# Optimization experiments

Measured on AMD Instinct MI355X. Metric: run time of the kernel, lower is better.

## Reference

```python
import jax, jax.numpy as jnp
import numpy as np
import math

B, LL, LP, H, C, S, T = 16, 512, 2048, 1024, 8192, 10, 4
PAD_TOKEN_ID = 2000
VAR_TOKEN_BASE = 2001


def _attend(q, k, v):
    # q: [b,q,h], k/v: [b,k,h]
    scores = jnp.einsum('bqh,bkh->bqk', q, k) / math.sqrt(float(q.shape[-1]))
    w = jax.nn.softmax(scores, axis=-1)
    return jnp.einsum('bqk,bkh->bqh', w, v)


def _gru_cell(x, h, Wih, Whh, bih, bhh):
    gi = x @ Wih + bih   # [B,3H], gate order r,z,n (torch GRUCell)
    gh = h @ Whh + bhh
    i_r, i_z, i_n = jnp.split(gi, 3, axis=-1)
    h_r, h_z, h_n = jnp.split(gh, 3, axis=-1)
    r = jax.nn.sigmoid(i_r + h_r)
    z = jax.nn.sigmoid(i_z + h_z)
    n = jnp.tanh(i_n + r * h_n)
    return (1.0 - z) * n + z * h


def setup_inputs() -> dict:
    key = jax.random.key(0)
    ks = jax.random.split(key, 18)
    def lin(k, i, o):
        return jax.random.normal(k, (i, o), jnp.float32) * 0.02
    return {
        'logic_hidden': jax.random.normal(ks[0], (B, LL, H), jnp.float32),
        'prompt_hidden': jax.random.normal(ks[1], (B, LP, H), jnp.float32),
        'codebook_emb': jax.random.normal(ks[2], (C, H), jnp.float32) * 0.02,
        'W_init': lin(ks[3], 2 * H, H),
        'W_pq': lin(ks[4], H, H),
        'W_pk': lin(ks[5], H, H),
        'W_pv': lin(ks[6], H, H),
        'slot_queries': jax.random.normal(ks[7], (S - 1, H), jnp.float32) * 0.02,
        'W_sq': lin(ks[8], H, H),
        'W_op': lin(ks[9], H, H),
        'W_gate': lin(ks[10], H, 1),
        'b_gate': jnp.zeros((1,), jnp.float32),
        'W_stop': lin(ks[11], 2 * H, 1),
        'b_stop': jnp.zeros((1,), jnp.float32),
        'gru_Wih': lin(ks[12], H, 3 * H),
        'gru_Whh': lin(ks[13], H, 3 * H),
        'gru_bih': jnp.zeros((3 * H,), jnp.float32),
        'gru_bhh': jnp.zeros((3 * H,), jnp.float32),
    }


def reference(logic_hidden, prompt_hidden, codebook_emb, W_init, W_pq, W_pk, W_pv,
              slot_queries, W_sq, W_op, W_gate, b_gate, W_stop, b_stop,
              gru_Wih, gru_Whh, gru_bih, gru_bhh):
    batch = logic_hidden.shape[0]
    prompt_summary = prompt_hidden.mean(axis=1)
    logic_summary = logic_hidden.mean(axis=1)
    state = jnp.tanh(jnp.concatenate([prompt_summary, logic_summary], axis=-1) @ W_init)
    pk = prompt_hidden @ W_pk   # [B,LP,H]
    pv = prompt_hidden @ W_pv
    cb_sq = jnp.sum(codebook_emb * codebook_emb, axis=-1)   # [C]
    slot_idx = jnp.arange(S - 1, dtype=jnp.int64)[None, :].repeat(batch, axis=0)

    summaries, stop_logits, stop_probs = [], [], []
    for _ in range(T):
        state_q = (state @ W_pq)[:, None, :]
        state_ctx = _attend(state_q, pk, pv)[:, 0, :]         # [B,H]
        op_pre = state_ctx @ W_op
        # squared euclidean distance to codebook without [B,C,H] diff tensor
        dist = (jnp.sum(op_pre * op_pre, axis=-1, keepdims=True)
                - 2.0 * (op_pre @ codebook_emb.T) + cb_sq[None, :])  # [B,C]
        op_logits = -dist
        op_idx = jnp.argmax(op_logits, axis=-1)               # [B]
        op_embedding = codebook_emb[op_idx]                   # [B,H]
        slot_seed = state_ctx[:, None, :] + slot_queries[None, :, :]   # [B,S-1,H]
        slot_q = slot_seed @ W_sq
        slot_tensors = _attend(slot_q, pk, pv)                # [B,S-1,H]
        slot_use_probs = jax.nn.sigmoid((slot_seed @ W_gate)[..., 0] + b_gate[0])  # [B,S-1]
        slot_mask = slot_use_probs >= 0.5
        # fallback if no slot selected anywhere in the batch (global check, as in torch)
        fb_mask = jax.nn.one_hot(jnp.argmax(slot_use_probs, axis=-1), S - 1, dtype=jnp.bool_)
        slot_mask = jnp.where(jnp.any(slot_mask), slot_mask, fb_mask)
        mf = slot_mask.astype(slot_tensors.dtype)
        slot_summary = jnp.sum(slot_tensors * mf[..., None], axis=1) / \
            jnp.clip(jnp.sum(mf, axis=-1, keepdims=True), 1.0)
        matrix_summary = jnp.tanh(op_embedding + slot_summary)
        stop_logit = (jnp.concatenate([state_ctx, matrix_summary], axis=-1) @ W_stop)[:, 0] + b_stop[0]
        summaries.append(matrix_summary)
        stop_logits.append(stop_logit)
        stop_probs.append(jax.nn.sigmoid(stop_logit))
        state = _gru_cell(matrix_summary, state, gru_Wih, gru_Whh, gru_bih, gru_bhh)

    stop_logits_t = jnp.stack(stop_logits, axis=1)   # [B,T]
    stop_probs_t = jnp.stack(stop_probs, axis=1)
    summary_stack = jnp.stack(summaries, axis=1)     # [B,T,H]
    stop_hits = stop_probs_t >= 0.5
    chain_lengths = jnp.argmax(stop_hits.astype(jnp.int64), axis=1) + 1
    chain_lengths = jnp.where(jnp.sum(stop_hits, axis=1) == 0,
                              jnp.full_like(chain_lengths, T), chain_lengths)
    return summary_stack, stop_logits_t, stop_probs_t, chain_lengths
```

## Files before the change

kernel.cpp:

```cpp
#include <hip/hip_runtime.h>


#define DINL __device__ __forceinline__

DINL float dot4(float4 a, float4 b) {
  return fmaf(a.x, b.x, fmaf(a.y, b.y, fmaf(a.z, b.z, a.w * b.w)));
}
DINL unsigned sortable(float f) {
  unsigned u = __float_as_uint(f);
  return (u & 0x80000000u) ? ~u : (u | 0x80000000u);
}
#define AXPY4(A, W, P) \
  { A.x = fmaf(W, P.x, A.x); A.y = fmaf(W, P.y, A.y); A.z = fmaf(W, P.z, A.z); A.w = fmaf(W, P.w, A.w); }
#define ADD4(A, V) { A.x += V.x; A.y += V.y; A.z += V.z; A.w += V.w; }

static constexpr int F_CBSQ  = 0;
static constexpr int F_STATE = 8192;
static constexpr int F_WQK   = 24576;
static constexpr int F_T1    = F_WQK + 1048576;
static constexpr int F_WFUSE = F_T1 + 1048576;
static constexpr int F_SQKCP = F_WFUSE + 2105344;
static constexpr int F_E     = F_SQKCP + 36928;
static constexpr int F_UN    = F_E + 294912;
static constexpr int F_PMP   = F_UN;
static constexpr int F_LMP   = F_PMP + 1048576;
static constexpr int F_MEAN  = F_LMP + 262144;
static constexpr int F_S2P   = F_MEAN + 32768;
static constexpr int F_WQKP  = F_UN;
static constexpr int F_T1P   = F_UN + 4194304;
static constexpr int F_WFP   = F_UN;
static constexpr int F_QS1   = F_UN;
static constexpr int F_LST   = F_QS1 + 131072;
static constexpr int F_CTX   = F_LST + 4096;
static constexpr int F_FWP   = F_CTX + 16384;
static constexpr int F_OPV   = F_FWP + 1052672;
static constexpr int F_OPMAX = F_OPV + 16384;
static constexpr int F_OPIDX = F_OPMAX + 16384;
static constexpr int F_GPRE  = F_OPIDX + 64;
static constexpr int F_GC    = F_GPRE + 64;
static constexpr int F_STOPA = F_GC + 64;
static constexpr int F_QSLB  = F_STOPA + 64;
static constexpr int F_LPS   = F_QSLB + 16384;
static constexpr int F_SSUM  = F_LPS + 4672;
static constexpr int F_MS    = F_SSUM + 16384;
static constexpr int F_GP    = F_MS + 16384;
static constexpr int F_K8P   = F_GP + 786432;
static constexpr int F_BIG   = F_K8P + 262144;

struct SG {
  const float* Bm;
  const float* Bg;
  const float* a0;
  float* out;
  int M, N, Ncore, NB, kslice, ksh, lda, ldb, ldo, mr;
  float scale;
};

template <int MR>
DINL void sgemm_body(const SG p, int bx, float* As) {
  const int t = threadIdx.x;
  const int ks = bx / p.NB, nb = bx % p.NB;
  const int kslice = p.kslice;
  const int kb = ks * kslice;
  const int tot = p.M * kslice;
  for (int idx = t; idx < tot; idx += 256) {
    const int m = idx >> p.ksh;
    const int kl = idx & (kslice - 1);
    As[(m << p.ksh) + kl] = p.a0[m * p.lda + kb + kl];
  }
  __syncthreads();
  const int nl = t & 63, mg = t >> 6;
  const int n = nb * 64 + nl;
  const bool nok = (n < p.N);
  float acc[MR];
#pragma unroll
  for (int i = 0; i < MR; i++) acc[i] = 0.f;
  const bool useg = nok && (n >= p.Ncore);
  const float* Bc = p.Bm + n;
  for (int k4 = 0; k4 < kslice; k4 += 4) {
    float bv[4];
#pragma unroll
    for (int u = 0; u < 4; u++) {
      bv[u] = 0.f;
      if (nok) bv[u] = useg ? p.Bg[kb + k4 + u] : Bc[(kb + k4 + u) * p.ldb];
    }
#pragma unroll
    for (int i = 0; i < MR; i++) {
      const int m = mg + 4 * i;
      if (MR == 4 || m < p.M) {
        const float4 av = *(const float4*)&As[(m << p.ksh) + k4];
        acc[i] = fmaf(av.x, bv[0], acc[i]);
        acc[i] = fmaf(av.y, bv[1], acc[i]);
        acc[i] = fmaf(av.z, bv[2], acc[i]);
        acc[i] = fmaf(av.w, bv[3], acc[i]);
      }
    }
  }
  if (nok) {
#pragma unroll
    for (int i = 0; i < MR; i++) {
      const int m = mg + 4 * i;
      if (MR == 4 || m < p.M) p.out[(ks * p.M + m) * p.ldo + n] = acc[i] * p.scale;
    }
  }
}

__global__ __launch_bounds__(256) void k_sgemm(SG p) {
  __shared__ __align__(16) float As[4352];
  if (p.mr == 4) sgemm_body<4>(p, blockIdx.x, As);
  else sgemm_body<7>(p, blockIdx.x, As);
}

DINL int sw4(int c) { return c ^ (((c >> 5) & 3) << 2); }

__global__ __launch_bounds__(256) void k_wgT(const float* __restrict__ A1,
                                             const float* __restrict__ B,
                                             float* __restrict__ C1P,
                                             const float* __restrict__ A2,
                                             float* __restrict__ C2P) {
  __shared__ __align__(16) float As[16 * 132], Bs[16 * 132];
  const int bx = blockIdx.x;
  const int which = bx >> 8;
  const int rem = bx & 255;
  const int ks = rem >> 6;
  const int tile = rem & 63;
  const int bi = tile >> 3, bj = tile & 7;
  const float* A = which ? A2 : A1;
  float* CP = (which ? C2P : C1P) + ks * 1048576;
  const int t = threadIdx.x;
  const int sr = t >> 2, q4 = t & 3;
  const int tr = (t >> 4) << 3, tc = (t & 15) << 3;
  const int stc0 = sw4(tc), stc1 = sw4(tc + 4);
  float acc[8][8];
#pragma unroll
  for (int i = 0; i < 8; i++)
#pragma unroll
    for (int j = 0; j < 8; j++) acc[i][j] = 0.f;

  const int k00 = ks * 256;
  for (int k0 = k00; k0 < k00 + 256; k0 += 16) {
    __syncthreads();
#pragma unroll
    for (int h = 0; h < 2; h++) {
      const int r = sr + h * 64;
      const float4 av = *(const float4*)&A[(bi * 128 + r) * 1024 + k0 + q4 * 4];
      const float4 bv = *(const float4*)&B[(bj * 128 + r) * 1024 + k0 + q4 * 4];
      As[(q4 * 4 + 0) * 132 + r] = av.x; As[(q4 * 4 + 1) * 132 + r] = av.y;
      As[(q4 * 4 + 2) * 132 + r] = av.z; As[(q4 * 4 + 3) * 132 + r] = av.w;
      const int swr = sw4(r);
      Bs[(q4 * 4 + 0) * 132 + swr] = bv.x; Bs[(q4 * 4 + 1) * 132 + swr] = bv.y;
      Bs[(q4 * 4 + 2) * 132 + swr] = bv.z; Bs[(q4 * 4 + 3) * 132 + swr] = bv.w;
    }
    __syncthreads();
#pragma unroll
    for (int kk = 0; kk < 16; kk++) {
      const float* ar = &As[kk * 132];
      const float* br = &Bs[kk * 132];
      const float4 a0 = *(const float4*)&ar[tr];
      const float4 a1 = *(const float4*)&ar[tr + 4];
      const float4 b0 = *(const float4*)&br[stc0];
      const float4 b1 = *(const float4*)&br[stc1];
      const float a[8] = {a0.x, a0.y, a0.z, a0.w, a1.x, a1.y, a1.z, a1.w};
      const float b[8] = {b0.x, b0.y, b0.z, b0.w, b1.x, b1.y, b1.z, b1.w};
#pragma unroll
      for (int i = 0; i < 8; i++)
#pragma unroll
        for (int j = 0; j < 8; j++) acc[i][j] = fmaf(a[i], b[j], acc[i][j]);
    }
  }
#pragma unroll
  for (int i = 0; i < 8; i++) {
    const int row = bi * 128 + tr + i;
    *(float4*)&CP[row * 1024 + bj * 128 + tc] =
        make_float4(acc[i][0], acc[i][1], acc[i][2], acc[i][3]);
    *(float4*)&CP[row * 1024 + bj * 128 + tc + 4] =
        make_float4(acc[i][4], acc[i][5], acc[i][6], acc[i][7]);
  }
}

__global__ __launch_bounds__(256) void k_combT(const float* __restrict__ C1P,
                                               const float* __restrict__ C2P,
                                               float* __restrict__ C1,
                                               float* __restrict__ C2, float scale) {
  const int bx = blockIdx.x;
  const int half = bx >> 12;
  const int i = ((bx & 4095) << 8) + threadIdx.x;
  const float* src = half ? C2P : C1P;
  float s = 0.f;
#pragma unroll
  for (int ks = 0; ks < 4; ks++) s += src[ks * 1048576 + i];
  (half ? C2 : C1)[i] = s * scale;
}

__global__ __launch_bounds__(256) void k_wgF(const float* __restrict__ Wpv,
                                             const float* __restrict__ Wop,
                                             const float* __restrict__ T1,
                                             float* __restrict__ CfP) {
  __shared__ __align__(16) float As[16 * 132], Bs[16 * 132];
  const int bx = blockIdx.x;
  const int ks = bx >> 7;
  const int rem = bx & 127;
  const int bi = rem >> 4, bj = rem & 15;
  const float* Bsrc = (bj < 8) ? (Wop + bj * 128) : (T1 + (bj - 8) * 128);
  float* CP = CfP + ks * 2105344;
  const int t = threadIdx.x;
  const int sr = t >> 2, q4 = t & 3;
  const int kkq = t >> 4, c8 = (t & 15) << 3;
  const int tr = (t >> 4) << 3, tc = (t & 15) << 3;
  const int stc0 = sw4(tc), stc1 = sw4(tc + 4);
  float acc[8][8];
#pragma unroll
  for (int i = 0; i < 8; i++)
#pragma unroll
    for (int j = 0; j < 8; j++) acc[i][j] = 0.f;

  const int k00 = ks * 256;
  for (int k0 = k00; k0 < k00 + 256; k0 += 16) {
    __syncthreads();
#pragma unroll
    for (int h = 0; h < 2; h++) {
      const int r = sr + h * 64;
      const float4 av = *(const float4*)&Wpv[(bi * 128 + r) * 1024 + k0 + q4 * 4];
      As[(q4 * 4 + 0) * 132 + r] = av.x; As[(q4 * 4 + 1) * 132 + r] = av.y;
      As[(q4 * 4 + 2) * 132 + r] = av.z; As[(q4 * 4 + 3) * 132 + r] = av.w;
    }
    {
      const float4 v0 = *(const float4*)&Bsrc[(k0 + kkq) * 1024 + c8];
      const float4 v1 = *(const float4*)&Bsrc[(k0 + kkq) * 1024 + c8 + 4];
      *(float4*)&Bs[kkq * 132 + sw4(c8)] = v0;
      *(float4*)&Bs[kkq * 132 + sw4(c8 + 4)] = v1;
    }
    __syncthreads();
#pragma unroll
    for (int kk = 0; kk < 16; kk++) {
      const float* ar = &As[kk * 132];
      const float* br = &Bs[kk * 132];
      const float4 a0 = *(const float4*)&ar[tr];
      const float4 a1 = *(const float4*)&ar[tr + 4];
      const float4 b0 = *(const float4*)&br[stc0];
      const float4 b1 = *(const float4*)&br[stc1];
      const float a[8] = {a0.x, a0.y, a0.z, a0.w, a1.x, a1.y, a1.z, a1.w};
      const float b[8] = {b0.x, b0.y, b0.z, b0.w, b1.x, b1.y, b1.z, b1.w};
#pragma unroll
      for (int i = 0; i < 8; i++)
#pragma unroll
        for (int j = 0; j < 8; j++) acc[i][j] = fmaf(a[i], b[j], acc[i][j]);
    }
  }
#pragma unroll
  for (int i = 0; i < 8; i++) {
    const int row = bi * 128 + tr + i;
    *(float4*)&CP[row * 2056 + bj * 128 + tc] =
        make_float4(acc[i][0], acc[i][1], acc[i][2], acc[i][3]);
    *(float4*)&CP[row * 2056 + bj * 128 + tc + 4] =
        make_float4(acc[i][4], acc[i][5], acc[i][6], acc[i][7]);
  }
}

__global__ __launch_bounds__(256) void k_combF(const float* __restrict__ CfP,
                                               float* __restrict__ Cf) {
  const int i2 = blockIdx.x * 256 + threadIdx.x;
  const int r = i2 >> 11, c = i2 & 2047;
  float s = 0.f;
#pragma unroll
  for (int ks = 0; ks < 4; ks++) s += CfP[ks * 2105344 + r * 2056 + c];
  Cf[r * 2056 + c] = s;
}

__global__ __launch_bounds__(256) void k_gs(const float* __restrict__ Wpv,
                                            const float* __restrict__ Wgate,
                                            const float* __restrict__ Wstop,
                                            float* __restrict__ Cf) {
  const int t = threadIdx.x;
  const int row = blockIdx.x * 16 + (t >> 4);
  const int lane = t & 15;
  const float* base = Wpv + row * 1024 + lane * 64;
  const float* gb = Wgate + lane * 64;
  const float* sb = Wstop + lane * 64;
  float g = 0.f, s = 0.f;
#pragma unroll 4
  for (int k = 0; k < 64; k += 4) {
    const float4 av = *(const float4*)&base[k];
    const float4 gv = *(const float4*)&gb[k];
    const float4 sv = *(const float4*)&sb[k];
    g += dot4(av, gv);
    s += dot4(av, sv);
  }
#pragma unroll
  for (int off = 8; off > 0; off >>= 1) {
    g += __shfl_xor(g, off);
    s += __shfl_xor(s, off);
  }
  if (lane == 0) {
    Cf[row * 2056 + 2048] = g;
    Cf[row * 2056 + 2049] = s;
  }
}

__global__ __launch_bounds__(512) void k_E(const float* __restrict__ prompt,
                                           const float* __restrict__ sqkcP,
                                           float* __restrict__ E) {
  __shared__ __align__(16) char qsm[36864];
  const int b = blockIdx.y, kc = blockIdx.x;
  const int t = threadIdx.x;
  for (int idx = t; idx < 9216; idx += 512) {
    const int j = idx >> 10, h = idx & 1023;
    float s = 0.f;
    for (int sp = 0; sp < 4; sp++) s += sqkcP[(sp * 9 + j) * 1025 + h];
    const int x = idx << 2;
    *(float*)(qsm + (x ^ (((x >> 7) & 7) << 4))) = s;
  }
  __syncthreads();
  const int w = t >> 6, l = t & 63;
  const int bxl = 64 * l;
  const int key = ((bxl >> 7) & 7) << 4;
  const int o0 = bxl ^ key, o1 = (bxl + 16) ^ key, o2 = (bxl + 32) ^ key, o3 = (bxl + 48) ^ key;
  const int k0 = kc * 64 + w * 8;
  const float* pbase = prompt + ((b * 2048 + k0) << 10) + 16 * l;
  for (int ki = 0; ki < 8; ki++) {
    const float4* pr = (const float4*)(pbase + (ki << 10));
    const float4 p0 = pr[0], p1 = pr[1], p2 = pr[2], p3 = pr[3];
    float sj[9];
#pragma unroll
    for (int j = 0; j < 9; j++) {
      const char* qp = qsm + (j << 12);
      sj[j] = dot4(*(const float4*)(qp + o0), p0) + dot4(*(const float4*)(qp + o1), p1) +
              dot4(*(const float4*)(qp + o2), p2) + dot4(*(const float4*)(qp + o3), p3);
    }
#pragma unroll
    for (int off = 32; off > 0; off >>= 1) {
#pragma unroll
      for (int j = 0; j < 9; j++) sj[j] += __shfl_xor(sj[j], off);
    }
    float wv = sj[0];
#pragma unroll
    for (int j = 1; j < 9; j++)
      if (l == j) wv = sj[j];
    if (l < 9) E[(b * 2048 + k0 + ki) * 9 + l] = __expf(wv);
  }
}

__global__ __launch_bounds__(256) void k_meanpsum(const float* __restrict__ src,
                                                  float* __restrict__ out, int rpc) {
  const int s = blockIdx.x, b = blockIdx.y, t = threadIdx.x;
  const int R = gridDim.x * rpc;
  const float4* base = (const float4*)src + (size_t)(b * R + s * rpc) * 256 + t;
  float4 acc = make_float4(0.f, 0.f, 0.f, 0.f);
#pragma unroll 4
  for (int r = 0; r < rpc; r++) {
    const float4 v = base[r * 256];
    ADD4(acc, v);
  }
  ((float4*)out)[((s * 16 + b) << 8) + t] = acc;
}

__global__ __launch_bounds__(256) void k_cbsq(const float* __restrict__ cbv,
                                              float* __restrict__ out) {
  const int c = blockIdx.x * 4 + (threadIdx.x >> 6);
  const int l = threadIdx.x & 63;
  const float4* cr = (const float4*)(cbv + (c << 10));
  float s = 0.f;
#pragma unroll
  for (int r = 0; r < 4; r++) {
    const float4 v = cr[4 * l + r];
    s += dot4(v, v);
  }
#pragma unroll
  for (int off = 32; off > 0; off >>= 1) s += __shfl_xor(s, off);
  if (l == 0) out[c] = s;
}

__global__ __launch_bounds__(256) void k_meancat(const float* __restrict__ pmp,
                                                 const float* __restrict__ lmp,
                                                 float* __restrict__ mean) {
  const int gi = blockIdx.x * 256 + threadIdx.x;
  const int b = gi >> 11, k = gi & 2047;
  float v = 0.f;
  if (k < 1024) {
    for (int s = 0; s < 64; s++) v += pmp[((s * 16 + b) << 10) + k];
    v *= (1.f / 2048.f);
  } else {
    const int kk = k - 1024;
    for (int s = 0; s < 16; s++) v += lmp[((s * 16 + b) << 10) + kk];
    v *= (1.f / 512.f);
  }
  mean[b * 2048 + k] = v;
}

__global__ __launch_bounds__(256) void k_s2b(const float* __restrict__ s2p,
                                             float* __restrict__ state) {
  const int gi = blockIdx.x * 256 + threadIdx.x;
  const int b = gi >> 10, h = gi & 1023;
  float s = 0.f;
  for (int si = 0; si < 8; si++) s += s2p[((si * 16 + b) << 10) + h];
  state[gi] = tanhf(s);
}


DINL void ph_qs1(int bx, char* smemc, const float* state, const float* Wqk,
                 float* outP) {
  float* As = (float*)smemc;
  const int t = threadIdx.x;
  const int ks = bx >> 4, nb = bx & 15;
  const int kb = ks * 128;
  for (int idx = t; idx < 2048; idx += 256)
    As[idx] = state[((idx >> 7) << 10) + kb + (idx & 127)];
  __syncthreads();
  const int nl = t & 63, mg = t >> 6;
  const int n = nb * 64 + nl;
  const float* Bc = Wqk + n;
  float acc[4] = {0.f, 0.f, 0.f, 0.f};
  for (int k4 = 0; k4 < 128; k4 += 4) {
    float bv[4];
#pragma unroll
    for (int u = 0; u < 4; u++) bv[u] = Bc[(kb + k4 + u) << 10];
#pragma unroll
    for (int i = 0; i < 4; i++) {
      const float4 av = *(const float4*)&As[((mg + 4 * i) << 7) + k4];
      acc[i] = fmaf(av.x, bv[0], acc[i]);
      acc[i] = fmaf(av.y, bv[1], acc[i]);
      acc[i] = fmaf(av.z, bv[2], acc[i]);
      acc[i] = fmaf(av.w, bv[3], acc[i]);
    }
  }
#pragma unroll
  for (int i = 0; i < 4; i++)
    outP[((ks * 16 + mg + 4 * i) << 10) + n] = acc[i];
}

DINL void ph_flash(int vb, const float* prompt, const float* qs1P,
                   float* accst, float* lst) {
  const int b = vb >> 6;
  const int w = threadIdx.x >> 6, l = threadIdx.x & 63;
  const int chunk = (vb & 63) * 4 + w;
  float4 q0 = make_float4(0.f, 0.f, 0.f, 0.f), q1 = q0, q2 = q0, q3 = q0;
#pragma unroll
  for (int s = 0; s < 8; s++) {
    const float4* qp = (const float4*)(qs1P + ((s * 16 + b) << 10) + 16 * l);
    ADD4(q0, qp[0]); ADD4(q1, qp[1]); ADD4(q2, qp[2]); ADD4(q3, qp[3]);
  }
  float4 acc[4];
#pragma unroll
  for (int r = 0; r < 4; r++) acc[r] = make_float4(0.f, 0.f, 0.f, 0.f);
  float lsum = 0.f;
  const float* pbase = prompt + ((b * 2048 + chunk * 8) << 10) + 16 * l;
#pragma unroll 2
  for (int k = 0; k < 8; k++) {
    const float4* pr = (const float4*)(pbase + (k << 10));
    const float4 p0 = pr[0], p1 = pr[1], p2 = pr[2], p3 = pr[3];
    float s = dot4(q0, p0) + dot4(q1, p1) + dot4(q2, p2) + dot4(q3, p3);
#pragma unroll
    for (int off = 32; off > 0; off >>= 1) s += __shfl_xor(s, off);
    const float wgt = __expf(s);
    lsum += wgt;
    AXPY4(acc[0], wgt, p0); AXPY4(acc[1], wgt, p1);
    AXPY4(acc[2], wgt, p2); AXPY4(acc[3], wgt, p3);
  }
  float* ob = accst + ((chunk * 16 + b) << 10) + 16 * l;
#pragma unroll
  for (int r = 0; r < 4; r++) ((float4*)ob)[r] = acc[r];
  if (l == 0) lst[chunk * 16 + b] = lsum;
}

DINL void ph_cst(int bx, char* smemc, const float* accst, const float* lst,
                 float* ctx) {
  float4* sred = (float4*)smemc;
  float* rinvp = (float*)(smemc + 4096);
  const int b = bx >> 4, hq = bx & 15;
  const int t = threadIdx.x;
  if (t < 64) {
    float s = 0.f;
    for (int c = t; c < 256; c += 64) s += lst[c * 16 + b];
#pragma unroll
    for (int off = 32; off > 0; off >>= 1) s += __shfl_xor(s, off);
    if (t == 0) rinvp[0] = 1.f / s;
  }
  const int h4 = hq * 16 + (t & 15);
  const int cp = t >> 4;
  float4 a = make_float4(0.f, 0.f, 0.f, 0.f);
#pragma unroll
  for (int ci = 0; ci < 16; ci++) {
    const int c = cp * 16 + ci;
    const float4 v = ((const float4*)accst)[((c * 16 + b) << 8) + h4];
    ADD4(a, v);
  }
  sred[t] = a;
  __syncthreads();
  if (t < 16) {
    float4 s = sred[t];
    for (int p2 = 1; p2 < 16; p2++) {
      const float4 v = sred[p2 * 16 + t];
      ADD4(s, v);
    }
    const float rinv = rinvp[0];
    s.x *= rinv; s.y *= rinv; s.z *= rinv; s.w *= rinv;
    ((float4*)ctx)[(b << 8) + hq * 16 + t] = s;
  }
}

DINL void ph_fw(int bx, char* smemc, const float* ctx, const float* wfuse,
                float* outp) {
  float* As = (float*)smemc;
  const int t = threadIdx.x;
  const int ks = bx / 33, nb = bx % 33;
  const int kb = ks * 64;
  for (int idx = t; idx < 1024; idx += 256)
    As[idx] = ctx[((idx >> 6) << 10) + kb + (idx & 63)];
  __syncthreads();
  const int nl = t & 63, mg = t >> 6;
  const int n = nb * 64 + nl;
  const bool nok = (n < 2050);
  const float* Bc = wfuse + n;
  float acc[4] = {0.f, 0.f, 0.f, 0.f};
  for (int k4 = 0; k4 < 64; k4 += 4) {
    float bv[4];
#pragma unroll
    for (int u = 0; u < 4; u++) bv[u] = nok ? Bc[(kb + k4 + u) * 2056] : 0.f;
#pragma unroll
    for (int i = 0; i < 4; i++) {
      const float4 av = *(const float4*)&As[((mg + 4 * i) << 6) + k4];
      acc[i] = fmaf(av.x, bv[0], acc[i]);
      acc[i] = fmaf(av.y, bv[1], acc[i]);
      acc[i] = fmaf(av.z, bv[2], acc[i]);
      acc[i] = fmaf(av.w, bv[3], acc[i]);
    }
  }
  if (nok) {
#pragma unroll
    for (int i = 0; i < 4; i++) outp[(ks * 16 + mg + 4 * i) * 2056 + n] = acc[i];
  }
}

DINL void ph_combw(int bx, const float* fwP, const float* sqkcP, float* opv,
                   float* qslb, float* gpre, float* gc, float* stopA) {
  const int t = threadIdx.x;
  if (bx < 64) {
    const int i = bx * 256 + t;
    const int b = i >> 10, h = i & 1023;
    float s = 0.f;
    for (int p = 0; p < 16; p++) s += fwP[(p * 16 + b) * 2056 + h];
    opv[i] = s;
  } else if (bx < 128) {
    const int i = (bx - 64) * 256 + t;
    const int b = i >> 10, h = i & 1023;
    float s = 0.f;
    for (int p = 0; p < 16; p++) s += fwP[(p * 16 + b) * 2056 + 1024 + h];
    qslb[i] = s;
  } else {
    if (t < 16) {
      float g = 0.f, sa = 0.f;
      for (int p = 0; p < 16; p++) {
        g += fwP[(p * 16 + t) * 2056 + 2048];
        sa += fwP[(p * 16 + t) * 2056 + 2049];
      }
      gpre[t] = g;
      stopA[t] = sa;
    } else if (t < 25) {
      const int j = t - 16;
      float g = 0.f;
      for (int sp = 0; sp < 4; sp++) g += sqkcP[(sp * 9 + j) * 1025 + 1024];
      gc[j] = g;
    }
  }
}

DINL void ph_slot(int vb, char* smemc, const float* prompt, const float* qslb,
// ... 224 lines not shown
  const int kb = ks * 128;
  for (int idx = t; idx < 2048; idx += 256) {
    const int m = idx >> 7, kl = idx & 127;
    float v;
    if (!half) {
      float s = 0.f;
      for (int p = 0; p < 16; p++) s += k8p[((p * 16 + m) << 10) + kb + kl];
      v = tanhf(s + cbv[(opidx[m] << 10) + kb + kl]);
      if (nb == 0) {
        ms[(m << 10) + kb + kl] = v;
        dout[(m << 12) + (it << 10) + kb + kl] = v;
      }
    } else {
      v = state[(m << 10) + kb + kl];
    }
    As[idx] = v;
  }
  __syncthreads();
  const int nl = t & 63, mg = t >> 6;
  const int n = nb * 64 + nl;
  const float* Bc = (half ? Whh : Wih) + n;
  float acc[4] = {0.f, 0.f, 0.f, 0.f};
  for (int k4 = 0; k4 < 128; k4 += 4) {
    float bv[4];
#pragma unroll
    for (int u = 0; u < 4; u++) bv[u] = Bc[(kb + k4 + u) * 3072];
#pragma unroll
    for (int i = 0; i < 4; i++) {
      const float4 av = *(const float4*)&As[((mg + 4 * i) << 7) + k4];
      acc[i] = fmaf(av.x, bv[0], acc[i]);
      acc[i] = fmaf(av.y, bv[1], acc[i]);
      acc[i] = fmaf(av.z, bv[2], acc[i]);
      acc[i] = fmaf(av.w, bv[3], acc[i]);
    }
  }
  float* outp = gpP + half * 3072;
#pragma unroll
  for (int i = 0; i < 4; i++) outp[(ks * 16 + mg + 4 * i) * 6144 + n] = acc[i];
}

DINL void ph_k9b(int bx, const float* gp, const float* bih, const float* bhh,
                 float* state, const float* stopA, const float* ms,
                 const float* Wstop, const float* bstop, float* dout, int it) {
  const int t = threadIdx.x;
  if (bx < 64) {
    const int gi = bx * 256 + t;
    const int b = gi >> 10, h = gi & 1023;
    float ir = 0.f, iz = 0.f, inn = 0.f, hr = 0.f, hz = 0.f, hn = 0.f;
    for (int s = 0; s < 8; s++) {
      const float* g = gp + (s * 16 + b) * 6144;
      ir += g[h]; iz += g[1024 + h]; inn += g[2048 + h];
      hr += g[3072 + h]; hz += g[4096 + h]; hn += g[5120 + h];
    }
    ir += bih[h]; iz += bih[1024 + h]; inn += bih[2048 + h];
    hr += bhh[h]; hz += bhh[1024 + h]; hn += bhh[2048 + h];
    const float r = 1.f / (1.f + __expf(-(ir + hr)));
    const float z = 1.f / (1.f + __expf(-(iz + hz)));
    const float n = tanhf(fmaf(r, hn, inn));
    const float hold = state[gi];
    state[gi] = (1.f - z) * n + z * hold;
  } else {
    const int wid = (bx - 64) * 4 + (t >> 6);
    const int l = t & 63;
    float p = 0.f;
    for (int i = 0; i < 16; i++) {
      const int h = l + (i << 6);
      p = fmaf(ms[(wid << 10) + h], Wstop[1024 + h], p);
    }
#pragma unroll
    for (int off = 32; off > 0; off >>= 1) p += __shfl_xor(p, off);
    if (l == 0) {
      const float lg = p + stopA[wid] + bstop[0];
      dout[65536 + wid * 4 + it] = lg;
      dout[65600 + wid * 4 + it] = 1.f / (1.f + __expf(-lg));
    }
  }
}

__global__ __launch_bounds__(256) void kf_qs1(const float* state, const float* Wqk, float* outP) {
  __shared__ __align__(16) char smem[8192];
  ph_qs1(blockIdx.x, smem, state, Wqk, outP);
}
__global__ __launch_bounds__(256) void kf_flash(const float* prompt, const float* qs1P,
                                                float* accst, float* lst) {
  ph_flash(blockIdx.x, prompt, qs1P, accst, lst);
}
__global__ __launch_bounds__(256) void kf_cst(const float* accst, const float* lst, float* ctx) {
  __shared__ __align__(16) char smem[4112];
  ph_cst(blockIdx.x, smem, accst, lst, ctx);
}
__global__ __launch_bounds__(256) void kf_fw(const float* ctx, const float* wfuse, float* outp) {
  __shared__ __align__(16) char smem[4096];
  ph_fw(blockIdx.x, smem, ctx, wfuse, outp);
}
__global__ __launch_bounds__(256) void kf_combw(const float* fwP, const float* sqkcP,
                                                float* opv, float* qslb, float* gpre,
                                                float* gc, float* stopA) {
  ph_combw(blockIdx.x, fwP, sqkcP, opv, qslb, gpre, gc, stopA);
}
__global__ __launch_bounds__(256) void k_slotcb(const float* prompt, const float* qslb,
                                                const float* E, float* accp, float* lpsum,
                                                const float* opv, const float* cbv,
                                                const float* cbsqv,
                                                unsigned long long* opmaxp) {
  __shared__ __align__(16) char smem[33024];
  const int bx = blockIdx.x;
  if (bx < 512) ph_slot(bx, smem, prompt, qslb, E, accp, lpsum);
  else ph_cb(bx - 512, smem, opv, cbv, cbsqv, opmaxp);
}
__global__ __launch_bounds__(256) void kf_k7(const float* accp, const float* lpsum,
                                             const float* gpre_g, const float* gc_g,
                                             const float* bgate,
                                             const unsigned long long* opmax,
                                             int* opidx, float* ssum) {
  __shared__ __align__(16) char smem[2304];
  ph_k7(blockIdx.x, smem, accp, lpsum, gpre_g, gc_g, bgate, opmax, opidx, ssum);
}
__global__ __launch_bounds__(256) void kf_k8p(const float* ssum, const float* Wpv, float* outP) {
  __shared__ __align__(16) char smem[4096];
  ph_k8p(blockIdx.x, smem, ssum, Wpv, outP);
}
__global__ __launch_bounds__(256) void kf_gru(const float* k8p, const int* opidx,
                                              const float* cbv, const float* state,
                                              const float* Wih, const float* Whh,
                                              float* gpP, float* ms, float* dout, int it) {
  __shared__ __align__(16) char smem[8192];
  ph_gru(blockIdx.x, smem, k8p, opidx, cbv, state, Wih, Whh, gpP, ms, dout, it);
}
__global__ __launch_bounds__(256) void kf_k9b(const float* gp, const float* bih,
                                              const float* bhh, float* state,
                                              const float* stopA, const float* ms,
                                              const float* Wstop, const float* bstop,
                                              float* dout, int it) {
  ph_k9b(blockIdx.x, gp, bih, bhh, state, stopA, ms, Wstop, bstop, dout, it);
}
__global__ void kf_k10(float* __restrict__ dout) {
  const int t = threadIdx.x;
  if (t < 16) {
    int cl = 4;
    for (int it = 0; it < 4; it++) {
      if (dout[65536 + t * 4 + it] >= 0.f) { cl = it + 1; break; }
    }
    dout[65664 + t] = (float)cl;
  }
}

static SG baseSG() {
  SG p;
  p.Bm = nullptr; p.Bg = nullptr; p.a0 = nullptr; p.out = nullptr;
  p.M = 16; p.N = 1024; p.Ncore = 1024;
  p.NB = 16; p.kslice = 64; p.ksh = 6;
  p.lda = 1024; p.ldb = 1024; p.ldo = 1024;
  p.mr = 4; p.scale = 1.f;
  return p;
}

extern "C" void kernel_launch(void* const* d_in, const int* in_sizes, int n_in,
                              void* d_out, int out_size, void* d_ws, size_t ws_size,
                              hipStream_t stream) {
  (void)in_sizes; (void)n_in; (void)out_size; (void)ws_size;
  const float* logic  = (const float*)d_in[0];
  const float* prompt = (const float*)d_in[1];
  const float* cbv    = (const float*)d_in[2];
  const float* W_init = (const float*)d_in[3];
  const float* W_pq   = (const float*)d_in[4];
  const float* W_pk   = (const float*)d_in[5];
  const float* W_pv   = (const float*)d_in[6];
  const float* slotq  = (const float*)d_in[7];
  const float* W_sq   = (const float*)d_in[8];
  const float* W_op   = (const float*)d_in[9];
  const float* W_gate = (const float*)d_in[10];
  const float* b_gate = (const float*)d_in[11];
  const float* W_stop = (const float*)d_in[12];
  const float* b_stop = (const float*)d_in[13];
  const float* Wih    = (const float*)d_in[14];
  const float* Whh    = (const float*)d_in[15];
  const float* bih    = (const float*)d_in[16];
  const float* bhh    = (const float*)d_in[17];
  float* out = (float*)d_out;
  float* w = (float*)d_ws;

  const float inv32 = 1.0f / 32.0f;

  k_meanpsum<<<dim3(64, 16), 256, 0, stream>>>(prompt, w + F_PMP, 32);
  k_meanpsum<<<dim3(16, 16), 256, 0, stream>>>(logic, w + F_LMP, 32);
  k_cbsq<<<2048, 256, 0, stream>>>(cbv, w + F_CBSQ);
  k_gs<<<64, 256, 0, stream>>>(W_pv, W_gate, W_stop, w + F_WFUSE);
  k_meancat<<<128, 256, 0, stream>>>(w + F_PMP, w + F_LMP, w + F_MEAN);
  {
    SG p = baseSG();
    p.a0 = w + F_MEAN; p.Bm = W_init; p.out = w + F_S2P;
    p.kslice = 256; p.ksh = 8; p.lda = 2048; p.NB = 16;
    k_sgemm<<<128, 256, 0, stream>>>(p);
  }
  k_s2b<<<64, 256, 0, stream>>>(w + F_S2P, w + F_STATE);
  k_wgT<<<512, 256, 0, stream>>>(W_pq, W_pk, w + F_WQKP, W_sq, w + F_T1P);
  k_combT<<<8192, 256, 0, stream>>>(w + F_WQKP, w + F_T1P, w + F_WQK, w + F_T1, inv32);
  {
    SG p = baseSG();
    p.a0 = slotq; p.Bm = w + F_T1; p.Bg = W_gate;
    p.M = 9; p.N = 1025; p.Ncore = 1024; p.NB = 17;
    p.kslice = 256; p.ksh = 8; p.out = w + F_SQKCP; p.ldo = 1025; p.mr = 7;
    k_sgemm<<<68, 256, 0, stream>>>(p);
  }
  k_E<<<dim3(32, 16), 512, 0, stream>>>(prompt, w + F_SQKCP, w + F_E);
  k_wgF<<<512, 256, 0, stream>>>(W_pv, W_op, w + F_T1, w + F_WFP);
  k_combF<<<8192, 256, 0, stream>>>(w + F_WFP, w + F_WFUSE);

  for (int it = 0; it < 4; ++it) {
    kf_qs1<<<128, 256, 0, stream>>>(w + F_STATE, w + F_WQK, w + F_QS1);
    kf_flash<<<1024, 256, 0, stream>>>(prompt, w + F_QS1, w + F_BIG, w + F_LST);
    kf_cst<<<256, 256, 0, stream>>>(w + F_BIG, w + F_LST, w + F_CTX);
    kf_fw<<<528, 256, 0, stream>>>(w + F_CTX, w + F_WFUSE, w + F_FWP);
    kf_combw<<<129, 256, 0, stream>>>(w + F_FWP, w + F_SQKCP, w + F_OPV,
                                      w + F_QSLB, w + F_GPRE, w + F_GC, w + F_STOPA);
    k_slotcb<<<1024, 256, 0, stream>>>(prompt, w + F_QSLB, w + F_E,
                                       w + F_BIG, w + F_LPS, w + F_OPV, cbv,
                                       w + F_CBSQ,
                                       (unsigned long long*)(w + F_OPMAX));
    kf_k7<<<65, 256, 0, stream>>>(w + F_BIG, w + F_LPS, w + F_GPRE, w + F_GC,
                                  b_gate, (const unsigned long long*)(w + F_OPMAX),
                                  (int*)(w + F_OPIDX), w + F_SSUM);
    kf_k8p<<<256, 256, 0, stream>>>(w + F_SSUM, W_pv, w + F_K8P);
    kf_gru<<<768, 256, 0, stream>>>(w + F_K8P, (const int*)(w + F_OPIDX), cbv,
                                    w + F_STATE, Wih, Whh, w + F_GP, w + F_MS,
                                    out, it);
    kf_k9b<<<68, 256, 0, stream>>>(w + F_GP, bih, bhh, w + F_STATE, w + F_STOPA,
                                   w + F_MS, W_stop, b_stop, out, it);
  }
  kf_k10<<<1, 64, 0, stream>>>(out);
}
```

Measured before the change: 900.9 us.

## Merge setup kernels into four multi-phase launches and reduce flash partials in-block

The setup kernels that can run together (weight GEMM partials, means, codebook norms, gate sums, combines, E) are merged into four launches that dispatch on block index ranges. The workspace gets non-aliased regions so the merged phases cannot overwrite each other's buffers. The flash kernel now sums its four waves' partial accumulators in shared memory before writing, which shrinks the partial buffer and the reduction work in kf_cst. This removes launch gaps and per-iteration global traffic, at the cost of mixed register and LDS usage per merged kernel and a larger workspace.

```diff
diff --git a/kernel.cpp b/kernel.cpp
--- a/kernel.cpp
+++ b/kernel.cpp
@@ -15,25 +15,25 @@
 #define ADD4(A, V) { A.x += V.x; A.y += V.y; A.z += V.z; A.w += V.w; }
 
 static constexpr int F_CBSQ  = 0;
-static constexpr int F_STATE = 8192;
-static constexpr int F_WQK   = 24576;
+static constexpr int F_STATE = F_CBSQ + 8192;
+static constexpr int F_WQK   = F_STATE + 16384;
 static constexpr int F_T1    = F_WQK + 1048576;
 static constexpr int F_WFUSE = F_T1 + 1048576;
 static constexpr int F_SQKCP = F_WFUSE + 2105344;
 static constexpr int F_E     = F_SQKCP + 36928;
-static constexpr int F_UN    = F_E + 294912;
-static constexpr int F_PMP   = F_UN;
+static constexpr int F_PMP   = F_E + 294912;
 static constexpr int F_LMP   = F_PMP + 1048576;
 static constexpr int F_MEAN  = F_LMP + 262144;
 static constexpr int F_S2P   = F_MEAN + 32768;
-static constexpr int F_WQKP  = F_UN;
-static constexpr int F_T1P   = F_UN + 4194304;
-static constexpr int F_WFP   = F_UN;
-static constexpr int F_QS1   = F_UN;
-static constexpr int F_LST   = F_QS1 + 131072;
-static constexpr int F_CTX   = F_LST + 4096;
+static constexpr int F_WQKP  = F_S2P + 131072;
+static constexpr int F_T1P   = F_WQKP + 4194304;
+static constexpr int F_WFP   = F_T1P + 4194304;
+static constexpr int F_QS1   = F_WFP + 8421376;
+static constexpr int F_ACCSM = F_QS1 + 131072;
+static constexpr int F_LSM   = F_ACCSM + 1048576;
+static constexpr int F_CTX   = F_LSM + 1024;
 static constexpr int F_FWP   = F_CTX + 16384;
-static constexpr int F_OPV   = F_FWP + 1052672;
+static constexpr int F_OPV   = F_FWP + 526336;
 static constexpr int F_OPMAX = F_OPV + 16384;
 static constexpr int F_OPIDX = F_OPMAX + 16384;
 static constexpr int F_GPRE  = F_OPIDX + 64;
@@ -45,7 +45,7 @@
 static constexpr int F_MS    = F_SSUM + 16384;
 static constexpr int F_GP    = F_MS + 16384;
 static constexpr int F_K8P   = F_GP + 786432;
-static constexpr int F_BIG   = F_K8P + 262144;
+static constexpr int F_ACCP  = F_K8P + 262144;
 
 struct SG {
   const float* Bm;
@@ -105,21 +105,13 @@
   }
 }
 
-__global__ __launch_bounds__(256) void k_sgemm(SG p) {
-  __shared__ __align__(16) float As[4352];
-  if (p.mr == 4) sgemm_body<4>(p, blockIdx.x, As);
-  else sgemm_body<7>(p, blockIdx.x, As);
-}
-
 DINL int sw4(int c) { return c ^ (((c >> 5) & 3) << 2); }
 
-__global__ __launch_bounds__(256) void k_wgT(const float* __restrict__ A1,
-                                             const float* __restrict__ B,
-                                             float* __restrict__ C1P,
-                                             const float* __restrict__ A2,
-                                             float* __restrict__ C2P) {
-  __shared__ __align__(16) float As[16 * 132], Bs[16 * 132];
-  const int bx = blockIdx.x;
+DINL void ph_wgT(int bx, float* sm, const float* __restrict__ A1,
+                 const float* __restrict__ B, float* __restrict__ C1P,
+                 const float* __restrict__ A2, float* __restrict__ C2P) {
+  float* As = sm;
+  float* Bs = sm + 2112;
   const int which = bx >> 8;
   const int rem = bx & 255;
   const int ks = rem >> 6;
@@ -178,26 +170,11 @@
   }
 }
 
-__global__ __launch_bounds__(256) void k_combT(const float* __restrict__ C1P,
-                                               const float* __restrict__ C2P,
-                                               float* __restrict__ C1,
-                                               float* __restrict__ C2, float scale) {
-  const int bx = blockIdx.x;
-  const int half = bx >> 12;
-  const int i = ((bx & 4095) << 8) + threadIdx.x;
-  const float* src = half ? C2P : C1P;
-  float s = 0.f;
-#pragma unroll
-  for (int ks = 0; ks < 4; ks++) s += src[ks * 1048576 + i];
-  (half ? C2 : C1)[i] = s * scale;
-}
-
-__global__ __launch_bounds__(256) void k_wgF(const float* __restrict__ Wpv,
-                                             const float* __restrict__ Wop,
-                                             const float* __restrict__ T1,
-                                             float* __restrict__ CfP) {
-  __shared__ __align__(16) float As[16 * 132], Bs[16 * 132];
-  const int bx = blockIdx.x;
+DINL void ph_wgF(int bx, float* sm, const float* __restrict__ Wpv,
+                 const float* __restrict__ Wop, const float* __restrict__ T1,
+                 float* __restrict__ CfP) {
+  float* As = sm;
+  float* Bs = sm + 2112;
   const int ks = bx >> 7;
   const int rem = bx & 127;
   const int bi = rem >> 4, bj = rem & 15;
@@ -257,22 +234,38 @@
   }
 }
 
-__global__ __launch_bounds__(256) void k_combF(const float* __restrict__ CfP,
-                                               float* __restrict__ Cf) {
-  const int i2 = blockIdx.x * 256 + threadIdx.x;
-  const int r = i2 >> 11, c = i2 & 2047;
+DINL void ph_meanpsum(int vb, const float* __restrict__ src,
+                      float* __restrict__ out, int R) {
+  const int s = vb >> 4, b = vb & 15, t = threadIdx.x;
+  const float4* base = (const float4*)src + (size_t)(b * R + s * 32) * 256 + t;
+  float4 acc = make_float4(0.f, 0.f, 0.f, 0.f);
+#pragma unroll 4
+  for (int r = 0; r < 32; r++) {
+    const float4 v = base[r * 256];
+    ADD4(acc, v);
+  }
+  ((float4*)out)[((s * 16 + b) << 8) + t] = acc;
+}
+
+DINL void ph_cbsq(int vb, const float* __restrict__ cbv, float* __restrict__ out) {
+  const int c = vb * 4 + (threadIdx.x >> 6);
+  const int l = threadIdx.x & 63;
+  const float4* cr = (const float4*)(cbv + (c << 10));
   float s = 0.f;
 #pragma unroll
-  for (int ks = 0; ks < 4; ks++) s += CfP[ks * 2105344 + r * 2056 + c];
-  Cf[r * 2056 + c] = s;
-}
-
-__global__ __launch_bounds__(256) void k_gs(const float* __restrict__ Wpv,
-                                            const float* __restrict__ Wgate,
-                                            const float* __restrict__ Wstop,
-                                            float* __restrict__ Cf) {
-  const int t = threadIdx.x;
-  const int row = blockIdx.x * 16 + (t >> 4);
+  for (int r = 0; r < 4; r++) {
+    const float4 v = cr[4 * l + r];
+    s += dot4(v, v);
+  }
+#pragma unroll
+  for (int off = 32; off > 0; off >>= 1) s += __shfl_xor(s, off);
+  if (l == 0) out[c] = s;
+}
+
+DINL void ph_gs(int vb, const float* __restrict__ Wpv, const float* __restrict__ Wgate,
+                const float* __restrict__ Wstop, float* __restrict__ Cf) {
+  const int t = threadIdx.x;
+  const int row = vb * 16 + (t >> 4);
   const int lane = t & 15;
   const float* base = Wpv + row * 1024 + lane * 64;
   const float* gb = Wgate + lane * 64;
@@ -297,83 +290,9 @@
   }
 }
 
-__global__ __launch_bounds__(512) void k_E(const float* __restrict__ prompt,
-                                           const float* __restrict__ sqkcP,
-                                           float* __restrict__ E) {
-  __shared__ __align__(16) char qsm[36864];
-  const int b = blockIdx.y, kc = blockIdx.x;
-  const int t = threadIdx.x;
-  for (int idx = t; idx < 9216; idx += 512) {
-    const int j = idx >> 10, h = idx & 1023;
-    float s = 0.f;
-    for (int sp = 0; sp < 4; sp++) s += sqkcP[(sp * 9 + j) * 1025 + h];
-    const int x = idx << 2;
-    *(float*)(qsm + (x ^ (((x >> 7) & 7) << 4))) = s;
-  }
-  __syncthreads();
-  const int w = t >> 6, l = t & 63;
-  const int bxl = 64 * l;
-  const int key = ((bxl >> 7) & 7) << 4;
-  const int o0 = bxl ^ key, o1 = (bxl + 16) ^ key, o2 = (bxl + 32) ^ key, o3 = (bxl + 48) ^ key;
-  const int k0 = kc * 64 + w * 8;
-  const float* pbase = prompt + ((b * 2048 + k0) << 10) + 16 * l;
-  for (int ki = 0; ki < 8; ki++) {
-    const float4* pr = (const float4*)(pbase + (ki << 10));
-    const float4 p0 = pr[0], p1 = pr[1], p2 = pr[2], p3 = pr[3];
-    float sj[9];
-#pragma unroll
-    for (int j = 0; j < 9; j++) {
-      const char* qp = qsm + (j << 12);
-      sj[j] = dot4(*(const float4*)(qp + o0), p0) + dot4(*(const float4*)(qp + o1), p1) +
-              dot4(*(const float4*)(qp + o2), p2) + dot4(*(const float4*)(qp + o3), p3);
-    }
-#pragma unroll
-    for (int off = 32; off > 0; off >>= 1) {
-#pragma unroll
-      for (int j = 0; j < 9; j++) sj[j] += __shfl_xor(sj[j], off);
-    }
-    float wv = sj[0];
-#pragma unroll
-    for (int j = 1; j < 9; j++)
-      if (l == j) wv = sj[j];
-    if (l < 9) E[(b * 2048 + k0 + ki) * 9 + l] = __expf(wv);
-  }
-}
-
-__global__ __launch_bounds__(256) void k_meanpsum(const float* __restrict__ src,
-                                                  float* __restrict__ out, int rpc) {
-  const int s = blockIdx.x, b = blockIdx.y, t = threadIdx.x;
-  const int R = gridDim.x * rpc;
-  const float4* base = (const float4*)src + (size_t)(b * R + s * rpc) * 256 + t;
-  float4 acc = make_float4(0.f, 0.f, 0.f, 0.f);
-#pragma unroll 4
-  for (int r = 0; r < rpc; r++) {
-    const float4 v = base[r * 256];
-    ADD4(acc, v);
-  }
-  ((float4*)out)[((s * 16 + b) << 8) + t] = acc;
-}
-
-__global__ __launch_bounds__(256) void k_cbsq(const float* __restrict__ cbv,
-                                              float* __restrict__ out) {
-  const int c = blockIdx.x * 4 + (threadIdx.x >> 6);
-  const int l = threadIdx.x & 63;
-  const float4* cr = (const float4*)(cbv + (c << 10));
-  float s = 0.f;
-#pragma unroll
-  for (int r = 0; r < 4; r++) {
-    const float4 v = cr[4 * l + r];
-    s += dot4(v, v);
-  }
-#pragma unroll
-  for (int off = 32; off > 0; off >>= 1) s += __shfl_xor(s, off);
-  if (l == 0) out[c] = s;
-}
-
-__global__ __launch_bounds__(256) void k_meancat(const float* __restrict__ pmp,
-                                                 const float* __restrict__ lmp,
-                                                 float* __restrict__ mean) {
-  const int gi = blockIdx.x * 256 + threadIdx.x;
+DINL void ph_meancat(int vb, const float* __restrict__ pmp,
+                     const float* __restrict__ lmp, float* __restrict__ mean) {
+  const int gi = vb * 256 + threadIdx.x;
   const int b = gi >> 11, k = gi & 2047;
   float v = 0.f;
   if (k < 1024) {
@@ -387,13 +306,111 @@
   mean[b * 2048 + k] = v;
 }
 
-__global__ __launch_bounds__(256) void k_s2b(const float* __restrict__ s2p,
-                                             float* __restrict__ state) {
-  const int gi = blockIdx.x * 256 + threadIdx.x;
+DINL void ph_combT(int vb, const float* __restrict__ C1P, const float* __restrict__ C2P,
+                   float* __restrict__ C1, float* __restrict__ C2, float scale) {
+  const int half = vb >> 12;
+  const int i = ((vb & 4095) << 8) + threadIdx.x;
+  const float* src = half ? C2P : C1P;
+  float s = 0.f;
+#pragma unroll
+  for (int ks = 0; ks < 4; ks++) s += src[ks * 1048576 + i];
+  (half ? C2 : C1)[i] = s * scale;
+}
+
+DINL void ph_combF(int vb, const float* __restrict__ CfP, float* __restrict__ Cf) {
+  const int i2 = vb * 256 + threadIdx.x;
+  const int r = i2 >> 11, c = i2 & 2047;
+  float s = 0.f;
+#pragma unroll
+  for (int ks = 0; ks < 4; ks++) s += CfP[ks * 2105344 + r * 2056 + c];
+  Cf[r * 2056 + c] = s;
+}
+
+DINL void ph_s2b(int vb, const float* __restrict__ s2p, float* __restrict__ state) {
+  const int gi = vb * 256 + threadIdx.x;
   const int b = gi >> 10, h = gi & 1023;
   float s = 0.f;
   for (int si = 0; si < 8; si++) s += s2p[((si * 16 + b) << 10) + h];
   state[gi] = tanhf(s);
+}
+
+DINL void ph_E(int vb, char* qsm, const float* __restrict__ prompt,
+               const float* __restrict__ sqkcP, float* __restrict__ E) {
+  const int kc = vb & 63, b = vb >> 6;
+  const int t = threadIdx.x;
+  for (int idx = t; idx < 9216; idx += 256) {
+    const int j = idx >> 10, h = idx & 1023;
+    float s = 0.f;
+    for (int sp = 0; sp < 4; sp++) s += sqkcP[(sp * 9 + j) * 1025 + h];
+    const int x = idx << 2;
+    *(float*)(qsm + (x ^ (((x >> 7) & 7) << 4))) = s;
+  }
+  __syncthreads();
+  const int w = t >> 6, l = t & 63;
+  const int bxl = 64 * l;
+  const int key = ((bxl >> 7) & 7) << 4;
+  const int o0 = bxl ^ key, o1 = (bxl + 16) ^ key, o2 = (bxl + 32) ^ key, o3 = (bxl + 48) ^ key;
+  const int k0 = kc * 32 + w * 8;
+  const float* pbase = prompt + ((b * 2048 + k0) << 10) + 16 * l;
+  for (int ki = 0; ki < 8; ki++) {
+    const float4* pr = (const float4*)(pbase + (ki << 10));
+    const float4 p0 = pr[0], p1 = pr[1], p2 = pr[2], p3 = pr[3];
+    float sj[9];
+#pragma unroll
+    for (int j = 0; j < 9; j++) {
+      const char* qp = qsm + (j << 12);
+      sj[j] = dot4(*(const float4*)(qp + o0), p0) + dot4(*(const float4*)(qp + o1), p1) +
+              dot4(*(const float4*)(qp + o2), p2) + dot4(*(const float4*)(qp + o3), p3);
+    }
+#pragma unroll
+    for (int off = 32; off > 0; off >>= 1) {
+#pragma unroll
+      for (int j = 0; j < 9; j++) sj[j] += __shfl_xor(sj[j], off);
+    }
+    float wv = sj[0];
+#pragma unroll
+    for (int j = 1; j < 9; j++)
+      if (l == j) wv = sj[j];
+    if (l < 9) E[(b * 2048 + k0 + ki) * 9 + l] = __expf(wv);
+  }
+}
+
+__global__ __launch_bounds__(256) void k_setup1(const float* prompt, const float* logic,
+                                                const float* cbv, const float* Wpv,
+                                                const float* Wgate, const float* Wstop,
+                                                const float* Wpq, const float* Wsq,
+                                                const float* Wpk, float* w) {
+  __shared__ __align__(16) float sm[4224];
+  const int bx = blockIdx.x;
+  if (bx < 512) ph_wgT(bx, sm, Wpq, Wpk, w + F_WQKP, Wsq, w + F_T1P);
+  else if (bx < 1536) ph_meanpsum(bx - 512, prompt, w + F_PMP, 2048);
+  else if (bx < 1792) ph_meanpsum(bx - 1536, logic, w + F_LMP, 512);
+  else if (bx < 3840) ph_cbsq(bx - 1792, cbv, w + F_CBSQ);
+  else ph_gs(bx - 3840, Wpv, Wgate, Wstop, w + F_WFUSE);
+}
+
+__global__ __launch_bounds__(256) void k_setup2(float* w, float scale) {
+  const int bx = blockIdx.x;
+  if (bx < 8192) ph_combT(bx, w + F_WQKP, w + F_T1P, w + F_WQK, w + F_T1, scale);
+  else ph_meancat(bx - 8192, w + F_PMP, w + F_LMP, w + F_MEAN);
+}
+
+__global__ __launch_bounds__(256) void k_setup3(SG pInit, SG pSqkc,
+                                                const float* Wpv, const float* Wop,
+                                                float* w) {
+  __shared__ __align__(16) float As[4352];
+  const int bx = blockIdx.x;
+  if (bx < 512) ph_wgF(bx, As, Wpv, Wop, w + F_T1, w + F_WFP);
+  else if (bx < 640) sgemm_body<4>(pInit, bx - 512, As);
+  else sgemm_body<7>(pSqkc, bx - 640, As);
+}
+
+__global__ __launch_bounds__(256) void k_setup4(const float* prompt, float* w) {
+  __shared__ __align__(16) char qsm[36864];
+  const int bx = blockIdx.x;
+  if (bx < 1024) ph_E(bx, qsm, prompt, w + F_SQKCP, w + F_E);
+  else if (bx < 9216) ph_combF(bx - 1024, w + F_WFP, w + F_WFUSE);
+  else ph_s2b(bx - 9216, w + F_S2P, w + F_STATE);
 }
 
 
@@ -428,11 +445,12 @@
     outP[((ks * 16 + mg + 4 * i) << 10) + n] = acc[i];
 }
 
-DINL void ph_flash(int vb, const float* prompt, const float* qs1P,
-                   float* accst, float* lst) {
-  const int b = vb >> 6;
-  const int w = threadIdx.x >> 6, l = threadIdx.x & 63;
-  const int chunk = (vb & 63) * 4 + w;
+DINL void ph_flash(int g, int b, char* smemc, const float* prompt,
+                   const float* qs1P, float* accsm, float* lsm) {
+  float* red = (float*)smemc;
+  float* lred = (float*)(smemc + 16384);
+  const int t = threadIdx.x;
+  const int w = t >> 6, l = t & 63;
   float4 q0 = make_float4(0.f, 0.f, 0.f, 0.f), q1 = q0, q2 = q0, q3 = q0;
 #pragma unroll
   for (int s = 0; s < 8; s++) {
@@ -443,7 +461,8 @@
 #pragma unroll
   for (int r = 0; r < 4; r++) acc[r] = make_float4(0.f, 0.f, 0.f, 0.f);
   float lsum = 0.f;
-  const float* pbase = prompt + ((b * 2048 + chunk * 8) << 10) + 16 * l;
+  const int k0 = g * 32 + w * 8;
+  const float* pbase = prompt + ((b * 2048 + k0) << 10) + 16 * l;
 #pragma unroll 2
   for (int k = 0; k < 8; k++) {
     const float4* pr = (const float4*)(pbase + (k << 10));
@@ -456,32 +475,38 @@
     AXPY4(acc[0], wgt, p0); AXPY4(acc[1], wgt, p1);
     AXPY4(acc[2], wgt, p2); AXPY4(acc[3], wgt, p3);
   }
-  float* ob = accst + ((chunk * 16 + b) << 10) + 16 * l;
-#pragma unroll
-  for (int r = 0; r < 4; r++) ((float4*)ob)[r] = acc[r];
-  if (l == 0) lst[chunk * 16 + b] = lsum;
-}
-
-DINL void ph_cst(int bx, char* smemc, const float* accst, const float* lst,
+  float4* myr = (float4*)(red + w * 1024 + 16 * l);
+  myr[0] = acc[0]; myr[1] = acc[1]; myr[2] = acc[2]; myr[3] = acc[3];
+  if (l == 0) lred[w] = lsum;
+  __syncthreads();
+  float4 s0 = *(float4*)(red + t * 4);
+  const float4 s1 = *(float4*)(red + 1024 + t * 4);
+  const float4 s2 = *(float4*)(red + 2048 + t * 4);
+  const float4 s3 = *(float4*)(red + 3072 + t * 4);
+  ADD4(s0, s1); ADD4(s0, s2); ADD4(s0, s3);
+  *(float4*)&accsm[((b * 64 + g) << 10) + t * 4] = s0;
+  if (t == 0) lsm[b * 64 + g] = lred[0] + lred[1] + lred[2] + lred[3];
+}
+
+DINL void ph_cst(int bx, char* smemc, const float* accsm, const float* lsm,
                  float* ctx) {
   float4* sred = (float4*)smemc;
   float* rinvp = (float*)(smemc + 4096);
   const int b = bx >> 4, hq = bx & 15;
   const int t = threadIdx.x;
   if (t < 64) {
-    float s = 0.f;
-    for (int c = t; c < 256; c += 64) s += lst[c * 16 + b];
+    float s = lsm[b * 64 + t];
 #pragma unroll
     for (int off = 32; off > 0; off >>= 1) s += __shfl_xor(s, off);
     if (t == 0) rinvp[0] = 1.f / s;
   }
   const int h4 = hq * 16 + (t & 15);
-  const int cp = t >> 4;
+  const int gp = t >> 4;
   float4 a = make_float4(0.f, 0.f, 0.f, 0.f);
 #pragma unroll
-  for (int ci = 0; ci < 16; ci++) {
-    const int c = cp * 16 + ci;
-    const float4 v = ((const float4*)accst)[((c * 16 + b) << 8) + h4];
+  for (int gi = 0; gi < 4; gi++) {
+    const int g = gp * 4 + gi;
+    const float4 v = ((const float4*)accsm)[((b * 64 + g) << 8) + h4];
     ADD4(a, v);
   }
   sred[t] = a;
@@ -872,12 +897,13 @@
   ph_qs1(blockIdx.x, smem, state, Wqk, outP);
 }
 __global__ __launch_bounds__(256) void kf_flash(const float* prompt, const float* qs1P,
-                                                float* accst, float* lst) {
-  ph_flash(blockIdx.x, prompt, qs1P, accst, lst);
-}
-__global__ __launch_bounds__(256) void kf_cst(const float* accst, const float* lst, float* ctx) {
+                                                float* accsm, float* lsm) {
+  __shared__ __align__(16) char smem[16416];
+  ph_flash(blockIdx.x, blockIdx.y, smem, prompt, qs1P, accsm, lsm);
+}
+__global__ __launch_bounds__(256) void kf_cst(const float* accsm, const float* lsm, float* ctx) {
   __shared__ __align__(16) char smem[4112];
-  ph_cst(blockIdx.x, smem, accst, lst, ctx);
+  ph_cst(blockIdx.x, smem, accsm, lsm, ctx);
 }
 __global__ __launch_bounds__(256) void kf_fw(const float* ctx, const float* wfuse, float* outp) {
   __shared__ __align__(16) char smem[4096];
@@ -933,16 +959,6 @@
     }
     dout[65664 + t] = (float)cl;
   }
-}
-
-static SG baseSG() {
-  SG p;
-  p.Bm = nullptr; p.Bg = nullptr; p.a0 = nullptr; p.out = nullptr;
-  p.M = 16; p.N = 1024; p.Ncore = 1024;
-  p.NB = 16; p.kslice = 64; p.ksh = 6;
-  p.lda = 1024; p.ldb = 1024; p.ldo = 1024;
-  p.mr = 4; p.scale = 1.f;
-  return p;
 }
 
 extern "C" void kernel_launch(void* const* d_in, const int* in_sizes, int n_in,
@@ -972,43 +988,39 @@
 
   const float inv32 = 1.0f / 32.0f;
 
-  k_meanpsum<<<dim3(64, 16), 256, 0, stream>>>(prompt, w + F_PMP, 32);
-  k_meanpsum<<<dim3(16, 16), 256, 0, stream>>>(logic, w + F_LMP, 32);
-  k_cbsq<<<2048, 256, 0, stream>>>(cbv, w + F_CBSQ);
-  k_gs<<<64, 256, 0, stream>>>(W_pv, W_gate, W_stop, w + F_WFUSE);
-  k_meancat<<<128, 256, 0, stream>>>(w + F_PMP, w + F_LMP, w + F_MEAN);
+  k_setup1<<<3904, 256, 0, stream>>>(prompt, logic, cbv, W_pv, W_gate, W_stop,
+                                     W_pq, W_sq, W_pk, w);
+  k_setup2<<<8320, 256, 0, stream>>>(w, inv32);
   {
-    SG p = baseSG();
-    p.a0 = w + F_MEAN; p.Bm = W_init; p.out = w + F_S2P;
-    p.kslice = 256; p.ksh = 8; p.lda = 2048; p.NB = 16;
-    k_sgemm<<<128, 256, 0, stream>>>(p);
-  }
-  k_s2b<<<64, 256, 0, stream>>>(w + F_S2P, w + F_STATE);
-  k_wgT<<<512, 256, 0, stream>>>(W_pq, W_pk, w + F_WQKP, W_sq, w + F_T1P);
-  k_combT<<<8192, 256, 0, stream>>>(w + F_WQKP, w + F_T1P, w + F_WQK, w + F_T1, inv32);
-  {
-    SG p = baseSG();
-    p.a0 = slotq; p.Bm = w + F_T1; p.Bg = W_gate;
-    p.M = 9; p.N = 1025; p.Ncore = 1024; p.NB = 17;
-    p.kslice = 256; p.ksh = 8; p.out = w + F_SQKCP; p.ldo = 1025; p.mr = 7;
-    k_sgemm<<<68, 256, 0, stream>>>(p);
-  }
-  k_E<<<dim3(32, 16), 512, 0, stream>>>(prompt, w + F_SQKCP, w + F_E);
-  k_wgF<<<512, 256, 0, stream>>>(W_pv, W_op, w + F_T1, w + F_WFP);
-  k_combF<<<8192, 256, 0, stream>>>(w + F_WFP, w + F_WFUSE);
+    SG pInit;
+    pInit.Bm = W_init; pInit.Bg = nullptr; pInit.a0 = w + F_MEAN;
+    pInit.out = w + F_S2P;
+    pInit.M = 16; pInit.N = 1024; pInit.Ncore = 1024; pInit.NB = 16;
+    pInit.kslice = 256; pInit.ksh = 8; pInit.lda = 2048; pInit.ldb = 1024;
+    pInit.ldo = 1024; pInit.mr = 4; pInit.scale = 1.f;
+    SG pSqkc;
+    pSqkc.Bm = w + F_T1; pSqkc.Bg = W_gate; pSqkc.a0 = slotq;
+    pSqkc.out = w + F_SQKCP;
+    pSqkc.M = 9; pSqkc.N = 1025; pSqkc.Ncore = 1024; pSqkc.NB = 17;
+    pSqkc.kslice = 256; pSqkc.ksh = 8; pSqkc.lda = 1024; pSqkc.ldb = 1024;
+    pSqkc.ldo = 1025; pSqkc.mr = 7; pSqkc.scale = 1.f;
+    k_setup3<<<708, 256, 0, stream>>>(pInit, pSqkc, W_pv, W_op, w);
+  }
+  k_setup4<<<9280, 256, 0, stream>>>(prompt, w);
 
   for (int it = 0; it < 4; ++it) {
     kf_qs1<<<128, 256, 0, stream>>>(w + F_STATE, w + F_WQK, w + F_QS1);
-    kf_flash<<<1024, 256, 0, stream>>>(prompt, w + F_QS1, w + F_BIG, w + F_LST);
-    kf_cst<<<256, 256, 0, stream>>>(w + F_BIG, w + F_LST, w + F_CTX);
+    kf_flash<<<dim3(64, 16), 256, 0, stream>>>(prompt, w + F_QS1,
+                                               w + F_ACCSM, w + F_LSM);
+    kf_cst<<<256, 256, 0, stream>>>(w + F_ACCSM, w + F_LSM, w + F_CTX);
     kf_fw<<<528, 256, 0, stream>>>(w + F_CTX, w + F_WFUSE, w + F_FWP);
     kf_combw<<<129, 256, 0, stream>>>(w + F_FWP, w + F_SQKCP, w + F_OPV,
                                       w + F_QSLB, w + F_GPRE, w + F_GC, w + F_STOPA);
     k_slotcb<<<1024, 256, 0, stream>>>(prompt, w + F_QSLB, w + F_E,
-                                       w + F_BIG, w + F_LPS, w + F_OPV, cbv,
+                                       w + F_ACCP, w + F_LPS, w + F_OPV, cbv,
                                        w + F_CBSQ,
                                        (unsigned long long*)(w + F_OPMAX));
-    kf_k7<<<65, 256, 0, stream>>>(w + F_BIG, w + F_LPS, w + F_GPRE, w + F_GC,
+    kf_k7<<<65, 256, 0, stream>>>(w + F_ACCP, w + F_LPS, w + F_GPRE, w + F_GC,
                                   b_gate, (const unsigned long long*)(w + F_OPMAX),
                                   (int*)(w + F_OPIDX), w + F_SSUM);
     kf_k8p<<<256, 256, 0, stream>>>(w + F_SSUM, W_pv, w + F_K8P);
```

Measured after the change: 798.6 us. -11.4%, faster.
